# Performance work log

Measured on AMD Instinct MI355X. Metric: run time of the kernel, lower is better.

## Reference

```python
import jax, jax.numpy as jnp
import numpy as np

B, N, IN_F, OUT_F, OP_D = 64, 96, 128, 128, 48
SKIP_IDX = 1
ATTN_SCALE = 1.0


def setup_inputs() -> dict:
    key = jax.random.key(0)
    ks = jax.random.split(key, 7)
    return {
        "inputs": jax.random.normal(ks[0], (B, N, IN_F), dtype=jnp.float32),
        "adj": jax.random.randint(ks[1], (B, N, N), 0, 5, dtype=jnp.int64),
        "op_emb": jax.random.normal(ks[2], (B, N, N, OP_D), dtype=jnp.float32),
        "weight": jax.random.normal(ks[3], (IN_F, OUT_F), dtype=jnp.float32) * (1.0 / np.sqrt(OUT_F)),
        "attn_w": jax.random.normal(ks[4], (OP_D, OUT_F), dtype=jnp.float32) * (1.0 / np.sqrt(OP_D)),
        "attn_b": jax.random.normal(ks[5], (OUT_F,), dtype=jnp.float32) * 0.01,
        "self_op_emb": jax.random.normal(ks[6], (OP_D,), dtype=jnp.float32),
    }


def reference(inputs, adj, op_emb, weight, attn_w, attn_b, self_op_emb):
    # support: [B, N, OUT_F]
    support = jnp.matmul(inputs, weight)
    n = adj.shape[-1]
    eye = jnp.eye(n, dtype=bool)  # [N, N]
    # plus_I: replace diagonal op embeddings with self_op_emb, add I to adj
    op_emb = jnp.where(eye[..., None], self_op_emb, op_emb)  # [B,N,N,OP_D]
    adj = adj + eye.astype(adj.dtype)
    # attention over op embeddings: [B,N,N,OUT_F]
    attn = jax.nn.sigmoid(jnp.matmul(op_emb, attn_w) + attn_b)
    attn = (adj != 0)[..., None].astype(attn.dtype) * attn * ATTN_SCALE
    # skip-connection edges get attention == 1
    is_skip = (adj == SKIP_IDX)[..., None].astype(attn.dtype)
    attn = is_skip + (1.0 - is_skip) * attn
    # processed_info = sum_j attn[b,i,j,:] * support[b,j,:]; residual = support
    processed_info = jnp.einsum("bijd,bjd->bid", attn, support)
    return processed_info + support
```

## Files before the change

kernel.cpp:

```cpp
#include <hip/hip_runtime.h>
#include <hip/hip_bf16.h>


#define B_ 64
#define N_ 96
#define F_ 128
#define D_ 48
#define G_ 12
#define NGRP (N_ / G_)

typedef __attribute__((ext_vector_type(8))) short short8;
typedef __attribute__((ext_vector_type(4))) float f32x4;

#if __has_builtin(__builtin_amdgcn_exp2f)
#define EXP2(x) __builtin_amdgcn_exp2f(x)
#else
#define EXP2(x) exp2f(x)
#endif

__device__ __forceinline__ void gload_lds16(const void* g, void* l) {
    __builtin_amdgcn_global_load_lds(
        (const __attribute__((address_space(1))) void*)g,
        (__attribute__((address_space(3))) void*)l, 16, 0, 0);
}

__device__ __forceinline__ size_t s2i(int b, int mt, int r, int lg, int fbp) {
    return ((((size_t)b * 6 + mt) * 4 + r) * 4 + lg) * 64 + fbp;
}

__device__ __forceinline__ unsigned bfbits(float x) {
    union { __hip_bfloat16 h; unsigned short u; } cv;
    cv.h = __float2bfloat16(x);
    return (unsigned)cv.u;
}

__global__ __launch_bounds__(256, 4) void support_kernel(
    const float* __restrict__ inputs, const float* __restrict__ weight,
    float2* __restrict__ S2)
{
    __shared__ float in_lds[16 * F_];
    const int tid = threadIdx.x;
    const int row0 = blockIdx.x * 16;
    ((float4*)in_lds)[tid]       = ((const float4*)(inputs + (size_t)row0 * F_))[tid];
    ((float4*)in_lds)[tid + 256] = ((const float4*)(inputs + (size_t)row0 * F_))[tid + 256];
    __syncthreads();
    const int rl = tid >> 4, f0 = (tid & 15) * 8;
    float acc[8] = {0.f,0.f,0.f,0.f,0.f,0.f,0.f,0.f};
    #pragma unroll 4
    for (int k = 0; k < F_; ++k) {
        const float a = in_lds[rl * F_ + k];
        const float4 w0 = *(const float4*)(weight + k * F_ + f0);
        const float4 w1 = *(const float4*)(weight + k * F_ + f0 + 4);
        acc[0] += a * w0.x; acc[1] += a * w0.y; acc[2] += a * w0.z; acc[3] += a * w0.w;
        acc[4] += a * w1.x; acc[5] += a * w1.y; acc[6] += a * w1.z; acc[7] += a * w1.w;
    }
    const int R = row0 + rl;
    const int b = R / N_, j = R - b * N_;
    const int mt = j >> 4, lg = (j >> 2) & 3, r = j & 3;
    #pragma unroll
    for (int q = 0; q < 4; ++q) {
        const int fbp = (f0 >> 1) + q;
        S2[s2i(b, mt, r, lg, fbp)] = make_float2(acc[2 * q], acc[2 * q + 1]);
    }
}

__global__ __launch_bounds__(512, 4) void fused_kernel(
    const float* __restrict__ op_emb,
    const unsigned* __restrict__ adjw,
    const float* __restrict__ attn_w,
    const float* __restrict__ attn_b,
    const float* __restrict__ self_op,
    const float2* __restrict__ S2,
    float* __restrict__ out)
{
    __shared__ __align__(16) float F32buf[2][N_ * D_];
    __shared__ __align__(16) unsigned short Atile[N_ * 64];
    __shared__ __align__(8)  float2 Ppart[4][16];

    const int tid  = threadIdx.x;
    const int lane = tid & 63;
    const int wid  = tid >> 6;
    const int wf   = wid & 3;
    const int wj   = wid >> 2;
    const int lg   = lane >> 4;
    const int lm   = lane & 15;
    const int fb   = wf * 32 + lm * 2;
    const int fbp  = wf * 16 + lm;

    const int blk = blockIdx.x;
    const int b   = blk / NGRP;
    const int grp = blk - b * NGRP;
    const int i0  = grp * G_;

    const float kNL2E = -1.44269504088896f;

    const unsigned probe = adjw[2 * lane + 1];
    const bool use32 = __any(probe != 0);

    auto issue_tile = [&](int i, int pb) {
        const char* gbase = (const char*)(op_emb + (size_t)(b * N_ + i) * N_ * D_);
        char* lbase = (char*)(&F32buf[pb][0]);
        #pragma unroll
        for (int c0 = 0; c0 < 3; ++c0) {
            const int c = wid + 8 * c0;
            if (c < 18) gload_lds16(gbase + c * 1024 + lane * 16, lbase + c * 1024);
        }
    };
    auto load_adj = [&](int i) -> int {
        int a = 0;
        if (tid < N_) {
            const size_t idx = (size_t)(b * N_ + i) * N_ + tid;
            a = use32 ? (int)adjw[idx] : (int)adjw[2 * idx];
            a += (tid == i) ? 1 : 0;
        }
        return a;
    };

    issue_tile(i0, 0);
    int adjreg = load_adj(i0);

    short8 bfrag[2][2];
    float  bbias[2];
    {
        const float2 bb = *(const float2*)(attn_b + fb);
        bbias[0] = bb.x * kNL2E;
        bbias[1] = bb.y * kNL2E;
        #pragma unroll
        for (int ks = 0; ks < 2; ++ks) {
            short8 v0, v1;
            #pragma unroll
            for (int e = 0; e < 8; ++e) {
                const int d = ks * 32 + lg * 8 + e;
                if (d < D_) {
                    const float2 w = *(const float2*)(attn_w + d * F_ + fb);
                    v0[e] = (short)bfbits(w.x * kNL2E);
                    v1[e] = (short)bfbits(w.y * kNL2E);
                } else {
                    const unsigned one = (d == D_) ? bfbits(1.0f) : 0u;
                    v0[e] = (short)one;
                    v1[e] = (short)one;
                }
            }
            bfrag[0][ks] = v0;
            bfrag[1][ks] = v1;
        }
    }

    float2 sfrag[3][4];
    #pragma unroll
    for (int s = 0; s < 3; ++s)
        #pragma unroll
        for (int r = 0; r < 4; ++r)
            sfrag[s][r] = S2[s2i(b, 3 * wj + s, r, lg, fbp)];

    for (int v = tid; v < N_ * 7; v += 512) {
        const int j = v / 7, q = v - 7 * j;
        const int byte = j * 128 + ((100 + q * 4) ^ ((j & 7) << 4));
        *(unsigned*)((char*)Atile + byte) = 0u;
    }

    __syncthreads();

    #pragma unroll 1
    for (int g = 0; g < G_; ++g) {
        const int cur = g & 1;
        const int i = i0 + g;

        int adjnext = 0;
        if (g + 1 < G_) {
            issue_tile(i + 1, cur ^ 1);
            adjnext = load_adj(i + 1);
        }

        #pragma unroll
        for (int s = 0; s < 3; ++s) {
            const int w = tid + s * 512;
            if (w < N_ * 12) {
                const int j = w / 12, c = w - 12 * j;
                float4 p;
                if (j == i) p = *(const float4*)(self_op + c * 4);
                else        p = *(const float4*)((const char*)(&F32buf[cur][0]) + 16 * w);
                const int byte = j * 128 + ((c * 8) ^ ((j & 7) << 4));
                *(uint2*)((char*)Atile + byte) =
                    make_uint2(bfbits(p.x) | (bfbits(p.y) << 16),
                               bfbits(p.z) | (bfbits(p.w) << 16));
            }
        }
        if (tid < N_) {
            const float off = (adjreg == 0) ? 126.f : ((adjreg == 1) ? -126.f : 0.f);
            const int byte = tid * 128 + (96 ^ ((tid & 7) << 4));
            *(unsigned*)((char*)Atile + byte) = bfbits(off);
        }
        asm volatile("s_waitcnt lgkmcnt(0)" ::: "memory");
        __builtin_amdgcn_s_barrier();

        float osum0 = 0.f, osum1 = 0.f;
        #pragma unroll
        for (int s = 0; s < 3; ++s) {
            const int mt  = 3 * wj + s;
            const int jr  = mt * 16 + lm;
            const int swz = (lm & 7) << 4;
            const char* base = (const char*)Atile + jr * 128;
            const short8 a0 = *(const short8*)(base + (( 0 + lg * 16) ^ swz));
            const short8 a1 = *(const short8*)(base + ((64 + lg * 16) ^ swz));
            f32x4 c0 = (f32x4){bbias[0], bbias[0], bbias[0], bbias[0]};
            f32x4 c1 = (f32x4){bbias[1], bbias[1], bbias[1], bbias[1]};
            c0 = __builtin_amdgcn_mfma_f32_16x16x32_bf16(a0, bfrag[0][0], c0, 0, 0, 0);
            c0 = __builtin_amdgcn_mfma_f32_16x16x32_bf16(a1, bfrag[0][1], c0, 0, 0, 0);
            c1 = __builtin_amdgcn_mfma_f32_16x16x32_bf16(a0, bfrag[1][0], c1, 0, 0, 0);
            c1 = __builtin_amdgcn_mfma_f32_16x16x32_bf16(a1, bfrag[1][1], c1, 0, 0, 0);
            #pragma unroll
            for (int r = 0; r < 4; ++r) {
                const float s0 = __builtin_amdgcn_rcpf(1.f + EXP2(c0[r]));
                const float s1 = __builtin_amdgcn_rcpf(1.f + EXP2(c1[r]));
                osum0 = __builtin_fmaf(s0, sfrag[s][r].x, osum0);
                osum1 = __builtin_fmaf(s1, sfrag[s][r].y, osum1);
            }
        }
        osum0 += __shfl_xor(osum0, 16);
        osum0 += __shfl_xor(osum0, 32);
        osum1 += __shfl_xor(osum1, 16);
        osum1 += __shfl_xor(osum1, 32);
        if (wj == 1 && lg == 0)
            Ppart[wf][lm] = make_float2(osum0, osum1);
        asm volatile("s_waitcnt lgkmcnt(0)" ::: "memory");
        __builtin_amdgcn_s_barrier();

        if (wj == 0 && lg == 0) {
            const float2 pp = Ppart[wf][lm];
            const float2 sr = S2[s2i(b, i >> 4, i & 3, (i >> 2) & 3, fbp)];
            float2 o;
            o.x = osum0 + pp.x + sr.x;
            o.y = osum1 + pp.y + sr.y;
            *(float2*)(out + (size_t)(b * N_ + i) * F_ + fb) = o;
        }

        asm volatile("s_waitcnt vmcnt(0)" ::: "memory");
        __builtin_amdgcn_s_barrier();
        adjreg = adjnext;
    }
}

extern "C" void kernel_launch(void* const* d_in, const int* in_sizes, int n_in,
                              void* d_out, int out_size, void* d_ws, size_t ws_size,
                              hipStream_t stream) {
    const float*    inputs  = (const float*)d_in[0];
    const unsigned* adjw    = (const unsigned*)d_in[1];
    const float*    op_emb  = (const float*)d_in[2];
    const float*    weight  = (const float*)d_in[3];
    const float*    attn_w  = (const float*)d_in[4];
    const float*    attn_b  = (const float*)d_in[5];
    const float*    self_op = (const float*)d_in[6];
    float* out = (float*)d_out;
    float2* S2 = (float2*)d_ws;

    support_kernel<<<(B_ * N_) / 16, 256, 0, stream>>>(inputs, weight, S2);
    fused_kernel<<<B_ * NGRP, 512, 0, stream>>>(op_emb, adjw, attn_w, attn_b, self_op,
                                                S2, out);
}
```

Baseline: 61.48 us.

## Defer output write to next iteration to drop a barrier; shrink row group

Removes one of the two per-row barriers by double-buffering the cross-wave partial sums and writing each row's output during the next iteration, with a final epilogue for the last row. Separately, the rows per block drop from 12 to 8, giving more blocks (768 vs 512), and the launch-bounds occupancy hint rises to 6. The intent is less barrier stalling and better CU fill. The trade-off is that each block amortizes the attn_w fragment and S2 setup over fewer rows, and the higher occupancy target may squeeze registers.

```diff
diff --git a/kernel.cpp b/kernel.cpp
--- a/kernel.cpp
+++ b/kernel.cpp
@@ -6,7 +6,7 @@
 #define N_ 96
 #define F_ 128
 #define D_ 48
-#define G_ 12
+#define G_ 8
 #define NGRP (N_ / G_)
 
 typedef __attribute__((ext_vector_type(8))) short short8;
@@ -64,7 +64,7 @@
     }
 }
 
-__global__ __launch_bounds__(512, 4) void fused_kernel(
+__global__ __launch_bounds__(512, 6) void fused_kernel(
     const float* __restrict__ op_emb,
     const unsigned* __restrict__ adjw,
     const float* __restrict__ attn_w,
@@ -75,7 +75,7 @@
 {
     __shared__ __align__(16) float F32buf[2][N_ * D_];
     __shared__ __align__(16) unsigned short Atile[N_ * 64];
-    __shared__ __align__(8)  float2 Ppart[4][16];
+    __shared__ __align__(8)  float2 Ppart[2][4][16];
 
     const int tid  = threadIdx.x;
     const int lane = tid & 63;
@@ -161,6 +161,8 @@
 
     __syncthreads();
 
+    float osum_prev0 = 0.f, osum_prev1 = 0.f;
+
     #pragma unroll 1
     for (int g = 0; g < G_; ++g) {
         const int cur = g & 1;
@@ -170,6 +172,16 @@
         if (g + 1 < G_) {
             issue_tile(i + 1, cur ^ 1);
             adjnext = load_adj(i + 1);
+        }
+
+        if (g > 0 && wj == 0 && lg == 0) {
+            const int ip = i - 1;
+            const float2 pp = Ppart[(g - 1) & 1][wf][lm];
+            const float2 sr = S2[s2i(b, ip >> 4, ip & 3, (ip >> 2) & 3, fbp)];
+            float2 o;
+            o.x = osum_prev0 + pp.x + sr.x;
+            o.y = osum_prev1 + pp.y + sr.y;
+            *(float2*)(out + (size_t)(b * N_ + ip) * F_ + fb) = o;
         }
 
         #pragma unroll
@@ -222,22 +234,23 @@
         osum1 += __shfl_xor(osum1, 16);
         osum1 += __shfl_xor(osum1, 32);
         if (wj == 1 && lg == 0)
-            Ppart[wf][lm] = make_float2(osum0, osum1);
-        asm volatile("s_waitcnt lgkmcnt(0)" ::: "memory");
-        __builtin_amdgcn_s_barrier();
-
-        if (wj == 0 && lg == 0) {
-            const float2 pp = Ppart[wf][lm];
-            const float2 sr = S2[s2i(b, i >> 4, i & 3, (i >> 2) & 3, fbp)];
-            float2 o;
-            o.x = osum0 + pp.x + sr.x;
-            o.y = osum1 + pp.y + sr.y;
-            *(float2*)(out + (size_t)(b * N_ + i) * F_ + fb) = o;
-        }
-
-        asm volatile("s_waitcnt vmcnt(0)" ::: "memory");
+            Ppart[g & 1][wf][lm] = make_float2(osum0, osum1);
+        osum_prev0 = osum0;
+        osum_prev1 = osum1;
+
+        asm volatile("s_waitcnt vmcnt(0) lgkmcnt(0)" ::: "memory");
         __builtin_amdgcn_s_barrier();
         adjreg = adjnext;
+    }
+
+    if (wj == 0 && lg == 0) {
+        const int ip = i0 + G_ - 1;
+        const float2 pp = Ppart[(G_ - 1) & 1][wf][lm];
+        const float2 sr = S2[s2i(b, ip >> 4, ip & 3, (ip >> 2) & 3, fbp)];
+        float2 o;
+        o.x = osum_prev0 + pp.x + sr.x;
+        o.y = osum_prev1 + pp.y + sr.y;
+        *(float2*)(out + (size_t)(b * N_ + ip) * F_ + fb) = o;
     }
 }
 
```

New measurement: 98.90 us. 60.9% more time.
